# Performance work log

Measured on AMD Instinct MI355X. Metric: run time of the kernel, lower is better.

The kernel has to match this reference:

```python
import jax, jax.numpy as jnp
import numpy as np

C = 64

def conv2d(x, w, b, pad):
    out = jax.lax.conv_general_dilated(x, w, (1, 1), [(pad, pad), (pad, pad)],
                                       dimension_numbers=('NCHW', 'OIHW', 'NCHW'))
    return out + b[None, :, None, None]


def deform_conv(x, w_off, b_off, w, b, pad):
    # Standard pure-pytorch DeformConv2d (offset conv is 3x3/pad1, sampling on
    # zero-padded input, p0 starts at 1, bilinear gather, then kxk weight contraction).
    ks = w.shape[-1]
    N = ks * ks
    B, Cc, H, W = x.shape
    off = conv2d(x, w_off, b_off, 1)                      # (B, 2N, H, W)
    xp = jnp.pad(x, ((0, 0), (0, 0), (pad, pad), (pad, pad))) if pad > 0 else x
    Hp, Wp = xp.shape[2], xp.shape[3]
    off = off.transpose(0, 2, 3, 1)                       # (B, H, W, 2N)
    r = jnp.arange(-(ks - 1) // 2, (ks - 1) // 2 + 1, dtype=x.dtype)
    pn_x = jnp.repeat(r, ks)                              # (N,) kernel row offsets (n = i*ks + j)
    pn_y = jnp.tile(r, ks)                                # (N,) kernel col offsets
    p0_x = jnp.arange(1, H + 1, dtype=x.dtype)[:, None, None]   # (H,1,1)
    p0_y = jnp.arange(1, W + 1, dtype=x.dtype)[:, None]         # (W,1)
    px = off[..., :N] + p0_x + pn_x                       # (B,H,W,N) sample rows
    py = off[..., N:] + p0_y + pn_y                       # (B,H,W,N) sample cols
    fx = jnp.floor(jax.lax.stop_gradient(px))
    fy = jnp.floor(jax.lax.stop_gradient(py))
    lt_x = jnp.clip(fx, 0, Hp - 1)
    lt_y = jnp.clip(fy, 0, Wp - 1)
    rb_x = jnp.clip(fx + 1, 0, Hp - 1)
    rb_y = jnp.clip(fy + 1, 0, Wp - 1)
    pxc = jnp.clip(px, 0, Hp - 1)
    pyc = jnp.clip(py, 0, Wp - 1)
    g_lt = (1 + (lt_x - pxc)) * (1 + (lt_y - pyc))
    g_rb = (1 - (rb_x - pxc)) * (1 - (rb_y - pyc))
    g_lb = (1 + (lt_x - pxc)) * (1 - (rb_y - pyc))
    g_rt = (1 - (rb_x - pxc)) * (1 + (lt_y - pyc))
    xpf = xp.reshape(B, Cc, Hp * Wp)

    def gather(qx, qy):
        idx = (qx * Wp + qy).astype(jnp.int32).reshape(B, 1, -1)
        g = jnp.take_along_axis(xpf, jnp.broadcast_to(idx, (B, Cc, idx.shape[-1])), axis=2)
        return g.reshape(B, Cc, H, W, N)

    x_off = (g_lt[:, None] * gather(lt_x, lt_y) +
             g_rb[:, None] * gather(rb_x, rb_y) +
             g_lb[:, None] * gather(lt_x, rb_y) +
             g_rt[:, None] * gather(rb_x, lt_y))          # (B,C,H,W,N)
    out = jnp.einsum('bchwn,ocn->bohw', x_off, w.reshape(w.shape[0], Cc, N))
    return out + b[None, :, None, None]


def setup_inputs() -> dict:
    key = jax.random.key(0)
    ks_list = [1, 3, 5]
    keys = jax.random.split(key, 32)
    inp = {'x': jax.random.normal(keys[0], (4, C, 96, 96), dtype=jnp.float32)}
    i = 1
    for ks in ks_list:
        N = ks * ks
        inp[f'wo{ks}'] = jax.random.normal(keys[i], (2 * N, C, 3, 3), dtype=jnp.float32) * 0.01; i += 1
        inp[f'bo{ks}'] = jax.random.normal(keys[i], (2 * N,), dtype=jnp.float32) * 0.01; i += 1
        inp[f'w{ks}'] = jax.random.normal(keys[i], (C, C, ks, ks), dtype=jnp.float32) * 0.05; i += 1
        inp[f'b{ks}'] = jax.random.normal(keys[i], (C,), dtype=jnp.float32) * 0.05; i += 1
        inp[f'wa{ks}'] = jax.random.normal(keys[i], (C, C, ks, ks), dtype=jnp.float32) * 0.05; i += 1
        inp[f'ba{ks}'] = jax.random.normal(keys[i], (C,), dtype=jnp.float32) * 0.05; i += 1
    return inp


def reference(x, wo1, bo1, w1, b1, wa1, ba1, wo3, bo3, w3, b3, wa3, ba3, wo5, bo5, w5, b5, wa5, ba5):
    lrelu = lambda t: jnp.where(t >= 0, t, 0.1 * t)
    x1 = lrelu(deform_conv(x, wo1, bo1, w1, b1, 0))
    x2 = lrelu(deform_conv(x, wo3, bo3, w3, b3, 1))
    x3 = lrelu(deform_conv(x, wo5, bo5, w5, b5, 2))
    msf = x1 + x2 + x3
    att = jax.nn.sigmoid(conv2d(msf, wa1, ba1, 0) + conv2d(msf, wa3, ba3, 1) + conv2d(msf, wa5, ba5, 2))
    return msf * att + msf
```

## Files before the change

kernel.cpp:

```cpp
#include <hip/hip_runtime.h>
#include <math.h>

constexpr int B = 4, C = 64, H = 96, W = 96, HW = H * W;

constexpr size_t OFF_OFFALL = 0;
constexpr size_t OFF_MSF    = OFF_OFFALL;
constexpr size_t OFF_X1     = OFF_OFFALL + (size_t)B*72*HW;
constexpr size_t OFF_X2     = OFF_X1  + (size_t)B*64*HW;
constexpr size_t OFF_X3A    = OFF_X2  + (size_t)B*64*HW;
constexpr size_t OFF_X3B    = OFF_X3A + (size_t)B*64*HW;
constexpr size_t OFF_X3C    = OFF_X3B + (size_t)B*64*HW;
constexpr size_t OFF_WOT    = OFF_X3C + (size_t)B*64*HW;
constexpr size_t OFF_BOALL  = OFF_WOT + (size_t)64*9*72;
constexpr size_t OFF_W1T    = OFF_BOALL + 72;
constexpr size_t OFF_W3T    = OFF_W1T + (size_t)64*64;
constexpr size_t OFF_W5T    = OFF_W3T + (size_t)9*64*64;
constexpr size_t OFF_WEFF   = OFF_W5T + (size_t)25*64*64;
constexpr size_t OFF_BEFF   = OFF_WEFF + (size_t)64*25*64;

__global__ void prep_all(const float* __restrict__ wo1, const float* __restrict__ bo1,
                         const float* __restrict__ wo3, const float* __restrict__ bo3,
                         const float* __restrict__ wo5, const float* __restrict__ bo5,
                         const float* __restrict__ w1, const float* __restrict__ w3,
                         const float* __restrict__ w5,
                         const float* __restrict__ wa1, const float* __restrict__ ba1,
                         const float* __restrict__ wa3, const float* __restrict__ ba3,
                         const float* __restrict__ wa5, const float* __restrict__ ba5,
                         float* __restrict__ woT, float* __restrict__ boAll,
                         float* __restrict__ w1T, float* __restrict__ w3T,
                         float* __restrict__ w5T,
                         float* __restrict__ weff, float* __restrict__ beff) {
  int idx = blockIdx.x * 256 + threadIdx.x;
  if (idx < 41472) {
    int ic = idx / (9 * 72), tap = (idx / 72) % 9, oc = idx % 72;
    float v = 0.f;
    if (oc < 2)       v = wo1[(oc * 64 + ic) * 9 + tap];
    else if (oc < 20) v = wo3[((oc - 2) * 64 + ic) * 9 + tap];
    else if (oc < 70) v = wo5[((oc - 20) * 64 + ic) * 9 + tap];
    woT[idx] = v;
  }
  if (idx < 72) boAll[idx] = idx < 2 ? bo1[idx] : idx < 20 ? bo3[idx - 2] : idx < 70 ? bo5[idx - 20] : 0.f;
  if (idx < 64) beff[idx] = ba1[idx] + ba3[idx] + ba5[idx];
  int i2 = idx - 41472;
  if (i2 >= 0 && i2 < 143360) {
    int seg = i2 >> 12, rem = i2 & 4095;
    int c = rem >> 6, o = rem & 63;
    if (seg < 1)       w1T[rem]                     = w1[o * 64 + c];
    else if (seg < 10) w3T[(seg - 1) * 4096 + rem]  = w3[(o * 64 + c) * 9 + (seg - 1)];
    else               w5T[(seg - 10) * 4096 + rem] = w5[(o * 64 + c) * 25 + (seg - 10)];
  }
  int i3 = idx - 41472 - 143360;
  if (i3 >= 0 && i3 < 102400) {
    int ic = i3 / 1600, tap = (i3 / 64) % 25, oc = i3 & 63;
    int kh = tap / 5, kw = tap % 5;
    float v = wa5[(oc * 64 + ic) * 25 + tap];
    if (kh >= 1 && kh <= 3 && kw >= 1 && kw <= 3)
      v += wa3[(oc * 64 + ic) * 9 + (kh - 1) * 3 + (kw - 1)];
    if (tap == 12) v += wa1[oc * 64 + ic];
    weff[i3] = v;
  }
}

__global__ __launch_bounds__(256) void conv_off(const float* __restrict__ x,
                                                const float* __restrict__ woT,
                                                const float* __restrict__ boAll,
                                                float* __restrict__ offAll) {
  __shared__ __align__(16) float xs[8][3][100];
  __shared__ __align__(16) float wsh[8 * 9 * 72];
  const int h = blockIdx.x, b = blockIdx.y;
  const int tid = threadIdx.x;
  const int ocg = tid >> 5, pixg = tid & 31;
  const int oc0 = ocg * 9, w0 = pixg * 3;
  float acc[9][3] = {};

  for (int cc = 0; cc < 8; ++cc) {
    __syncthreads();
    for (int idx = tid; idx < 2400; idx += 256) {
      int ic = idx / 300;
      int r  = (idx / 100) % 3;
      int j  = idx % 100;
      int wc = j - 1, hr = h - 1 + r;
      float v = 0.f;
      if (wc >= 0 && wc < 96 && hr >= 0 && hr < 96)
        v = x[((size_t)(b * 64 + cc * 8 + ic) * 96 + hr) * 96 + wc];
      xs[ic][r][j] = v;
    }
    {
      const float4* src = reinterpret_cast<const float4*>(woT + cc * 5184);
      float4* dst = reinterpret_cast<float4*>(wsh);
      for (int i = tid; i < 1296; i += 256) dst[i] = src[i];
    }
    __syncthreads();
#pragma unroll 2
    for (int ic = 0; ic < 8; ++ic) {
#pragma unroll
      for (int kh = 0; kh < 3; ++kh) {
        float xv[5];
#pragma unroll
        for (int t = 0; t < 5; ++t) xv[t] = xs[ic][kh][w0 + t];
#pragma unroll
        for (int kw = 0; kw < 3; ++kw) {
          const float* wrow = &wsh[(ic * 9 + kh * 3 + kw) * 72 + oc0];
#pragma unroll
          for (int o = 0; o < 9; ++o) {
            float wv = wrow[o];
            acc[o][0] += wv * xv[kw + 0];
            acc[o][1] += wv * xv[kw + 1];
            acc[o][2] += wv * xv[kw + 2];
          }
        }
      }
    }
  }
#pragma unroll
  for (int o = 0; o < 9; ++o) {
    int oc = oc0 + o;
    float bias = boAll[oc];
#pragma unroll
    for (int p = 0; p < 3; ++p)
      offAll[((size_t)(b * 72 + oc) * 96 + h) * 96 + w0 + p] = acc[o][p] + bias;
  }
}

template <int KS>
__device__ __forceinline__ void deform_body(const float* __restrict__ x,
                                            const float* __restrict__ offAll,
                                            const float* __restrict__ wT,
                                            float* __restrict__ dst,
                                            int n0, int n1,
                                            float* __restrict__ xoffn,
                                            float* __restrict__ wn,
                                            int* __restrict__ sp_i,
                                            float* __restrict__ sp_g,
                                            int h, int b, int tid) {
  constexpr int N = KS * KS, P = (KS - 1) / 2, HP = H + 2 * P;
  constexpr int CHB = (KS == 1) ? 0 : (KS == 3) ? 2 : 20;
  const int ocg = tid >> 5, pixg = tid & 31;
  const int oc0 = ocg * 8, w0 = pixg * 3;
  float acc[8][3] = {};
  const float* xb = x + (size_t)b * 64 * HW;

  for (int n = n0; n < n1; ++n) {
    if (tid < 96) {
      int w = tid;
      float ox = offAll[((size_t)(b * 72 + CHB + n) * 96 + h) * 96 + w];
      float oy = offAll[((size_t)(b * 72 + CHB + N + n) * 96 + h) * 96 + w];
      float px = ox + (float)(h + 1 + n / KS - P);
      float py = oy + (float)(w + 1 + n % KS - P);
      float fx = floorf(px), fy = floorf(py);
      float hpm = (float)(HP - 1);
      float ltx = fminf(fmaxf(fx, 0.f), hpm);
      float rbx = fminf(fmaxf(fx + 1.f, 0.f), hpm);
      float lty = fminf(fmaxf(fy, 0.f), hpm);
      float rby = fminf(fmaxf(fy + 1.f, 0.f), hpm);
      float pxc = fminf(fmaxf(px, 0.f), hpm);
      float pyc = fminf(fmaxf(py, 0.f), hpm);
      float gx0 = 1.f + (ltx - pxc);
      float gx1 = 1.f - (rbx - pxc);
      float gy0 = 1.f + (lty - pyc);
      float gy1 = 1.f - (rby - pyc);
      sp_i[0 * 96 + w] = (int)ltx; sp_i[1 * 96 + w] = (int)rbx;
      sp_i[2 * 96 + w] = (int)lty; sp_i[3 * 96 + w] = (int)rby;
      sp_g[0 * 96 + w] = gx0 * gy0;
      sp_g[1 * 96 + w] = gx1 * gy1;
      sp_g[2 * 96 + w] = gx0 * gy1;
      sp_g[3 * 96 + w] = gx1 * gy0;
    }
    __syncthreads();
    for (int cc = 0; cc < 2; ++cc) {
      {
        const float4* src = reinterpret_cast<const float4*>(wT + (size_t)n * 4096 + cc * 2048);
        float4* dw = reinterpret_cast<float4*>(wn);
        dw[tid] = src[tid];
        dw[tid + 256] = src[tid + 256];
      }
#pragma unroll 4
      for (int it = 0; it < 12; ++it) {
        int idx = it * 256 + tid;
        int cl = idx / 96, rp = idx - cl * 96;
        int ix0 = sp_i[0 * 96 + rp], ix1 = sp_i[1 * 96 + rp];
        int iy0 = sp_i[2 * 96 + rp], iy1 = sp_i[3 * 96 + rp];
        const float* xc = xb + (size_t)(cc * 32 + cl) * HW;
        float v00, v11, v01, v10;
        if constexpr (P == 0) {
          v00 = xc[ix0 * 96 + iy0];
          v11 = xc[ix1 * 96 + iy1];
          v01 = xc[ix0 * 96 + iy1];
          v10 = xc[ix1 * 96 + iy0];
        } else {
          int rx0 = ix0 - P, rx1 = ix1 - P, ry0 = iy0 - P, ry1 = iy1 - P;
          bool bx0 = (rx0 >= 0) && (rx0 < 96), bx1 = (rx1 >= 0) && (rx1 < 96);
          bool by0 = (ry0 >= 0) && (ry0 < 96), by1 = (ry1 >= 0) && (ry1 < 96);
          v00 = (bx0 && by0) ? xc[rx0 * 96 + ry0] : 0.f;
          v11 = (bx1 && by1) ? xc[rx1 * 96 + ry1] : 0.f;
          v01 = (bx0 && by1) ? xc[rx0 * 96 + ry1] : 0.f;
          v10 = (bx1 && by0) ? xc[rx1 * 96 + ry0] : 0.f;
        }
        xoffn[idx] = sp_g[0 * 96 + rp] * v00 + sp_g[1 * 96 + rp] * v11 +
                     sp_g[2 * 96 + rp] * v01 + sp_g[3 * 96 + rp] * v10;
      }
      __syncthreads();
#pragma unroll 2
      for (int cl = 0; cl < 32; ++cl) {
        float xv0 = xoffn[cl * 96 + w0];
        float xv1 = xoffn[cl * 96 + w0 + 1];
        float xv2 = xoffn[cl * 96 + w0 + 2];
        const float4* wp = reinterpret_cast<const float4*>(wn + cl * 64 + oc0);
        float4 wa = wp[0], wb = wp[1];
        float wv[8] = {wa.x, wa.y, wa.z, wa.w, wb.x, wb.y, wb.z, wb.w};
#pragma unroll
        for (int o = 0; o < 8; ++o) {
          acc[o][0] += wv[o] * xv0;
          acc[o][1] += wv[o] * xv1;
          acc[o][2] += wv[o] * xv2;
        }
      }
      __syncthreads();
    }
  }
#pragma unroll
  for (int o = 0; o < 8; ++o) {
    int oc = oc0 + o;
    size_t base = ((size_t)(b * 64 + oc) * 96 + h) * 96 + w0;
    dst[base + 0] = acc[o][0];
    dst[base + 1] = acc[o][1];
    dst[base + 2] = acc[o][2];
  }
}

__global__ __launch_bounds__(256, 6) void deform_all(const float* __restrict__ x,
                                                     const float* __restrict__ offAll,
                                                     const float* __restrict__ w1T,
                                                     const float* __restrict__ w3T,
                                                     const float* __restrict__ w5T,
                                                     float* __restrict__ x1,
                                                     float* __restrict__ x2,
                                                     float* __restrict__ x3a,
                                                     float* __restrict__ x3b,
                                                     float* __restrict__ x3c) {
  __shared__ __align__(16) float xoffn[32 * 96];
  __shared__ __align__(16) float wn[32 * 64];
  __shared__ int   sp_i[4 * 96];
  __shared__ float sp_g[4 * 96];
  int bid = blockIdx.x;
  int typ = bid & 3, idx = bid >> 2;
  int h = idx % 96, b = idx / 96;
  int tid = threadIdx.x;
  if (typ == 0)      deform_body<5>(x, offAll, w5T, x3a, 0, 9,  xoffn, wn, sp_i, sp_g, h, b, tid);
  else if (typ == 1) deform_body<5>(x, offAll, w5T, x3b, 9, 17, xoffn, wn, sp_i, sp_g, h, b, tid);
  else if (typ == 2) deform_body<5>(x, offAll, w5T, x3c, 17, 25, xoffn, wn, sp_i, sp_g, h, b, tid);
  else {
    deform_body<3>(x, offAll, w3T, x2, 0, 9, xoffn, wn, sp_i, sp_g, h, b, tid);
    deform_body<1>(x, offAll, w1T, x1, 0, 1, xoffn, wn, sp_i, sp_g, h, b, tid);
  }
}

__global__ __launch_bounds__(256) void msf_build(const float* __restrict__ x1,
                                                 const float* __restrict__ x2,
                                                 const float* __restrict__ x3a,
                                                 const float* __restrict__ x3b,
                                                 const float* __restrict__ x3c,
                                                 const float* __restrict__ b1,
                                                 const float* __restrict__ b3,
                                                 const float* __restrict__ b5,
                                                 float* __restrict__ msf) {
  int i = blockIdx.x * 256 + threadIdx.x;
  int c = (i / 2304) & 63;
  float bb1 = b1[c], bb3 = b3[c], bb5 = b5[c];
  float4 v1 = reinterpret_cast<const float4*>(x1)[i];
  float4 v2 = reinterpret_cast<const float4*>(x2)[i];
  float4 va = reinterpret_cast<const float4*>(x3a)[i];
  float4 vb = reinterpret_cast<const float4*>(x3b)[i];
  float4 vc = reinterpret_cast<const float4*>(x3c)[i];
  float4 m;
  {
    float a1 = v1.x + bb1; a1 = a1 >= 0.f ? a1 : 0.1f * a1;
    float a2 = v2.x + bb3; a2 = a2 >= 0.f ? a2 : 0.1f * a2;
    float a3 = va.x + vb.x + vc.x + bb5; a3 = a3 >= 0.f ? a3 : 0.1f * a3;
    m.x = a1 + a2 + a3;
  }
  {
    float a1 = v1.y + bb1; a1 = a1 >= 0.f ? a1 : 0.1f * a1;
    float a2 = v2.y + bb3; a2 = a2 >= 0.f ? a2 : 0.1f * a2;
    float a3 = va.y + vb.y + vc.y + bb5; a3 = a3 >= 0.f ? a3 : 0.1f * a3;
    m.y = a1 + a2 + a3;
  }
  {
    float a1 = v1.z + bb1; a1 = a1 >= 0.f ? a1 : 0.1f * a1;
    float a2 = v2.z + bb3; a2 = a2 >= 0.f ? a2 : 0.1f * a2;
    float a3 = va.z + vb.z + vc.z + bb5; a3 = a3 >= 0.f ? a3 : 0.1f * a3;
    m.z = a1 + a2 + a3;
  }
  {
    float a1 = v1.w + bb1; a1 = a1 >= 0.f ? a1 : 0.1f * a1;
    float a2 = v2.w + bb3; a2 = a2 >= 0.f ? a2 : 0.1f * a2;
    float a3 = va.w + vb.w + vc.w + bb5; a3 = a3 >= 0.f ? a3 : 0.1f * a3;
    m.w = a1 + a2 + a3;
  }
  reinterpret_cast<float4*>(msf)[i] = m;
}

__global__ __launch_bounds__(128, 2) void att_final(const float* __restrict__ msf,
                                                    const float* __restrict__ weff,
                                                    const float* __restrict__ beff,
                                                    float* __restrict__ out) {
  __shared__ __align__(16) float xs[4 * 5 * 100];
  __shared__ __align__(16) float wsh[4 * 25 * 32];
  const int h = blockIdx.x, b = blockIdx.y, zoc = blockIdx.z * 32;
  const int tid = threadIdx.x;
  const int ocg = tid >> 5, colg = tid & 31;
  const int oc0 = ocg * 8, w0 = colg * 3;
  float acc[8][3] = {};

  for (int cc = 0; cc < 16; ++cc) {
    __syncthreads();
    for (int idx = tid; idx < 2000; idx += 128) {
      int ic = idx / 500, r = (idx / 100) % 5, j = idx % 100;
      int hr = h - 2 + r, wc = j - 2;
      float v = 0.f;
      if (hr >= 0 && hr < 96 && wc >= 0 && wc < 96)
        v = msf[((size_t)(b * 64 + cc * 4 + ic) * 96 + hr) * 96 + wc];
      xs[idx] = v;
    }
    for (int i = tid; i < 800; i += 128) {
      int ict = i >> 3, o4 = i & 7;
      int ic = ict / 25, tap = ict % 25;
      reinterpret_cast<float4*>(wsh)[i] =
          *reinterpret_cast<const float4*>(weff + ((size_t)(cc * 4 + ic) * 25 + tap) * 64 + zoc + o4 * 4);
    }
    __syncthreads();
#pragma unroll
    for (int ic = 0; ic < 4; ++ic) {
#pragma unroll
      for (int kh = 0; kh < 5; ++kh) {
        float xv[7];
#pragma unroll
        for (int t = 0; t < 7; ++t) xv[t] = xs[ic * 500 + kh * 100 + w0 + t];
#pragma unroll
        for (int kw = 0; kw < 5; ++kw) {
          const float4* wp = reinterpret_cast<const float4*>(&wsh[(ic * 25 + kh * 5 + kw) * 32 + oc0]);
          float4 wa = wp[0], wb = wp[1];
          float wv[8] = {wa.x, wa.y, wa.z, wa.w, wb.x, wb.y, wb.z, wb.w};
#pragma unroll
          for (int o = 0; o < 8; ++o) {
            acc[o][0] += wv[o] * xv[kw + 0];
            acc[o][1] += wv[o] * xv[kw + 1];
            acc[o][2] += wv[o] * xv[kw + 2];
          }
        }
      }
    }
  }
#pragma unroll
  for (int o = 0; o < 8; ++o) {
    int oc = zoc + oc0 + o;
    float bz = beff[oc];
#pragma unroll
    for (int p = 0; p < 3; ++p) {
      float z = acc[o][p] + bz;
      float att = 1.f / (1.f + __expf(-z));
      size_t oi = ((size_t)(b * 64 + oc) * 96 + h) * 96 + w0 + p;
      float m = msf[oi];
      out[oi] = m + m * att;
    }
  }
}

extern "C" void kernel_launch(void* const* d_in, const int* in_sizes, int n_in,
                              void* d_out, int out_size, void* d_ws, size_t ws_size,
                              hipStream_t stream) {
  const float* x   = (const float*)d_in[0];
  const float* wo1 = (const float*)d_in[1];
  const float* bo1 = (const float*)d_in[2];
  const float* w1  = (const float*)d_in[3];
  const float* b1  = (const float*)d_in[4];
  const float* wa1 = (const float*)d_in[5];
  const float* ba1 = (const float*)d_in[6];
  const float* wo3 = (const float*)d_in[7];
  const float* bo3 = (const float*)d_in[8];
  const float* w3  = (const float*)d_in[9];
  const float* b3  = (const float*)d_in[10];
  const float* wa3 = (const float*)d_in[11];
  const float* ba3 = (const float*)d_in[12];
  const float* wo5 = (const float*)d_in[13];
  const float* bo5 = (const float*)d_in[14];
  const float* w5  = (const float*)d_in[15];
  const float* b5  = (const float*)d_in[16];
  const float* wa5 = (const float*)d_in[17];
  const float* ba5 = (const float*)d_in[18];

  float* ws     = (float*)d_ws;
  float* offAll = ws + OFF_OFFALL;
  float* msf    = ws + OFF_MSF;
  float* x1     = ws + OFF_X1;
  float* x2     = ws + OFF_X2;
  float* x3a    = ws + OFF_X3A;
  float* x3b    = ws + OFF_X3B;
  float* x3c    = ws + OFF_X3C;
  float* woT    = ws + OFF_WOT;
  float* boAll  = ws + OFF_BOALL;
  float* w1T    = ws + OFF_W1T;
  float* w3T    = ws + OFF_W3T;
  float* w5T    = ws + OFF_W5T;
  float* weff   = ws + OFF_WEFF;
  float* beff   = ws + OFF_BEFF;

  float* out = (float*)d_out;

  hipLaunchKernelGGL(prep_all, dim3(1122), dim3(256), 0, stream,
                     wo1, bo1, wo3, bo3, wo5, bo5, w1, w3, w5,
                     wa1, ba1, wa3, ba3, wa5, ba5,
                     woT, boAll, w1T, w3T, w5T, weff, beff);
  hipLaunchKernelGGL(conv_off, dim3(96, 4), dim3(256), 0, stream, x, woT, boAll, offAll);
  hipLaunchKernelGGL(deform_all, dim3(1536), dim3(256), 0, stream,
                     x, offAll, w1T, w3T, w5T, x1, x2, x3a, x3b, x3c);
  hipLaunchKernelGGL(msf_build, dim3(2304), dim3(256), 0, stream,
                     x1, x2, x3a, x3b, x3c, b1, b3, b5, msf);
  hipLaunchKernelGGL(att_final, dim3(96, 4, 2), dim3(128), 0, stream,
                     msf, weff, beff, out);
}
```

Measured before the change: 750.2 us.

## Move deformable conv contraction to split-bf16 MFMA with padded input and atomics

Replaces the scalar FMA weight contraction in the deformable conv kernels with bf16 MFMA 16x16x32 instructions. Both activations and weights are split into high and low bf16 parts and combined with three MFMAs to keep close to fp32 accuracy. The input is pre-padded into a 100x100 buffer so the bilinear gathers need no bounds checks. The 5x5 branch accumulates its three tap slices atomically into one zeroed buffer instead of three separate buffers. Offset-conv and attention kernels are also split across more blocks along output channels, and the work adds extra pad and zero kernels plus atomic traffic.

```diff
diff --git a/kernel.cpp b/kernel.cpp
--- a/kernel.cpp
+++ b/kernel.cpp
@@ -2,20 +2,23 @@
 #include <math.h>
 
 constexpr int B = 4, C = 64, H = 96, W = 96, HW = H * W;
+constexpr int HWP = 100 * 100;
+
+typedef __attribute__((ext_vector_type(8))) short bf16x8;
+typedef __attribute__((ext_vector_type(4))) float f32x4;
+typedef __attribute__((ext_vector_type(4))) unsigned int uint4v;
 
 constexpr size_t OFF_OFFALL = 0;
-constexpr size_t OFF_MSF    = OFF_OFFALL;
 constexpr size_t OFF_X1     = OFF_OFFALL + (size_t)B*72*HW;
 constexpr size_t OFF_X2     = OFF_X1  + (size_t)B*64*HW;
-constexpr size_t OFF_X3A    = OFF_X2  + (size_t)B*64*HW;
-constexpr size_t OFF_X3B    = OFF_X3A + (size_t)B*64*HW;
-constexpr size_t OFF_X3C    = OFF_X3B + (size_t)B*64*HW;
-constexpr size_t OFF_WOT    = OFF_X3C + (size_t)B*64*HW;
+constexpr size_t OFF_X3     = OFF_X2  + (size_t)B*64*HW;
+constexpr size_t OFF_XPAD   = OFF_X3  + (size_t)B*64*HW;
+constexpr size_t OFF_MSF    = OFF_XPAD;
+constexpr size_t OFF_WOT    = OFF_XPAD + (size_t)B*64*HWP;
 constexpr size_t OFF_BOALL  = OFF_WOT + (size_t)64*9*72;
-constexpr size_t OFF_W1T    = OFF_BOALL + 72;
-constexpr size_t OFF_W3T    = OFF_W1T + (size_t)64*64;
-constexpr size_t OFF_W5T    = OFF_W3T + (size_t)9*64*64;
-constexpr size_t OFF_WEFF   = OFF_W5T + (size_t)25*64*64;
+constexpr size_t OFF_WPKH   = OFF_BOALL + 128;
+constexpr size_t OFF_WPKL   = OFF_WPKH + 71680;
+constexpr size_t OFF_WEFF   = OFF_WPKL + 71680;
 constexpr size_t OFF_BEFF   = OFF_WEFF + (size_t)64*25*64;
 
 __global__ void prep_all(const float* __restrict__ wo1, const float* __restrict__ bo1,
@@ -27,8 +30,7 @@
                          const float* __restrict__ wa3, const float* __restrict__ ba3,
                          const float* __restrict__ wa5, const float* __restrict__ ba5,
                          float* __restrict__ woT, float* __restrict__ boAll,
-                         float* __restrict__ w1T, float* __restrict__ w3T,
-                         float* __restrict__ w5T,
+                         unsigned short* __restrict__ wPkH, unsigned short* __restrict__ wPkL,
                          float* __restrict__ weff, float* __restrict__ beff) {
   int idx = blockIdx.x * 256 + threadIdx.x;
   if (idx < 41472) {
@@ -41,15 +43,7 @@
   }
   if (idx < 72) boAll[idx] = idx < 2 ? bo1[idx] : idx < 20 ? bo3[idx - 2] : idx < 70 ? bo5[idx - 20] : 0.f;
   if (idx < 64) beff[idx] = ba1[idx] + ba3[idx] + ba5[idx];
-  int i2 = idx - 41472;
-  if (i2 >= 0 && i2 < 143360) {
-    int seg = i2 >> 12, rem = i2 & 4095;
-    int c = rem >> 6, o = rem & 63;
-    if (seg < 1)       w1T[rem]                     = w1[o * 64 + c];
-    else if (seg < 10) w3T[(seg - 1) * 4096 + rem]  = w3[(o * 64 + c) * 9 + (seg - 1)];
-    else               w5T[(seg - 10) * 4096 + rem] = w5[(o * 64 + c) * 25 + (seg - 10)];
-  }
-  int i3 = idx - 41472 - 143360;
+  int i3 = idx - 41472;
   if (i3 >= 0 && i3 < 102400) {
     int ic = i3 / 1600, tap = (i3 / 64) % 25, oc = i3 & 63;
     int kh = tap / 5, kw = tap % 5;
@@ -59,36 +53,69 @@
     if (tap == 12) v += wa1[oc * 64 + ic];
     weff[i3] = v;
   }
-}
-
-__global__ __launch_bounds__(256) void conv_off(const float* __restrict__ x,
-                                                const float* __restrict__ woT,
-                                                const float* __restrict__ boAll,
-                                                float* __restrict__ offAll) {
-  __shared__ __align__(16) float xs[8][3][100];
-  __shared__ __align__(16) float wsh[8 * 9 * 72];
-  const int h = blockIdx.x, b = blockIdx.y;
-  const int tid = threadIdx.x;
+  int e = idx - 143872;
+  if (e >= 0 && e < 143360) {
+    int i  = e & 7;
+    int l  = (e >> 3) & 63;
+    int nt = (e >> 9) & 3;
+    int kt = (e >> 11) & 1;
+    int tap = e >> 12;
+    int c  = kt * 32 + 8 * (l >> 4) + i;
+    int oc = nt * 16 + (l & 15);
+    float w;
+    if (tap == 0)      w = w1[oc * 64 + c];
+    else if (tap < 10) w = w3[(oc * 64 + c) * 9 + (tap - 1)];
+    else               w = w5[(oc * 64 + c) * 25 + (tap - 10)];
+    unsigned bits = __float_as_uint(w);
+    unsigned hib  = bits & 0xffff0000u;
+    float lo = w - __uint_as_float(hib);
+    wPkH[e] = (unsigned short)(bits >> 16);
+    wPkL[e] = (unsigned short)(__float_as_uint(lo) >> 16);
+  }
+}
+
+__global__ void pad_x(const float* __restrict__ x, float* __restrict__ xpad) {
+  int i = blockIdx.x * 256 + threadIdx.x;
+  if (i >= B * 64 * HWP) return;
+  int u = i % HWP, bc = i / HWP;
+  int r = u / 100, col = u % 100;
+  float v = 0.f;
+  if (r >= 2 && r < 98 && col >= 2 && col < 98)
+    v = x[(size_t)bc * HW + (r - 2) * 96 + (col - 2)];
+  xpad[i] = v;
+}
+
+__global__ void zero_buf(float* __restrict__ p) {
+  int i = blockIdx.x * 256 + threadIdx.x;
+  reinterpret_cast<float4*>(p)[i] = make_float4(0.f, 0.f, 0.f, 0.f);
+}
+
+template <int NOC, int OCB>
+__device__ __forceinline__ void conv_off_body(const float* __restrict__ x,
+                                              const float* __restrict__ woT,
+                                              const float* __restrict__ boAll,
+                                              float* __restrict__ offAll,
+                                              float* __restrict__ xs,
+                                              float* __restrict__ wsh,
+                                              int h, int b, int tid) {
+  constexpr int OCPG = NOC / 8;
   const int ocg = tid >> 5, pixg = tid & 31;
-  const int oc0 = ocg * 9, w0 = pixg * 3;
-  float acc[9][3] = {};
+  const int oc0 = ocg * OCPG, w0 = pixg * 3;
+  float acc[OCPG][3] = {};
 
   for (int cc = 0; cc < 8; ++cc) {
     __syncthreads();
     for (int idx = tid; idx < 2400; idx += 256) {
-      int ic = idx / 300;
-      int r  = (idx / 100) % 3;
-      int j  = idx % 100;
+      int ic = idx / 300, r = (idx / 100) % 3, j = idx % 100;
       int wc = j - 1, hr = h - 1 + r;
       float v = 0.f;
       if (wc >= 0 && wc < 96 && hr >= 0 && hr < 96)
         v = x[((size_t)(b * 64 + cc * 8 + ic) * 96 + hr) * 96 + wc];
-      xs[ic][r][j] = v;
-    }
-    {
-      const float4* src = reinterpret_cast<const float4*>(woT + cc * 5184);
-      float4* dst = reinterpret_cast<float4*>(wsh);
-      for (int i = tid; i < 1296; i += 256) dst[i] = src[i];
+      xs[(ic * 3 + r) * 100 + j] = v;
+    }
+    for (int i = tid; i < 8 * 9 * NOC; i += 256) {
+      int ic = i / (9 * NOC), rem = i % (9 * NOC), tap = rem / NOC, j = rem % NOC;
+      wsh[i] = woT[((size_t)(cc * 8 + ic) * 9 + tap) * 72 + OCB + j];
     }
     __syncthreads();
 #pragma unroll 2
@@ -97,12 +124,12 @@
       for (int kh = 0; kh < 3; ++kh) {
         float xv[5];
 #pragma unroll
-        for (int t = 0; t < 5; ++t) xv[t] = xs[ic][kh][w0 + t];
+        for (int t = 0; t < 5; ++t) xv[t] = xs[(ic * 3 + kh) * 100 + w0 + t];
 #pragma unroll
         for (int kw = 0; kw < 3; ++kw) {
-          const float* wrow = &wsh[(ic * 9 + kh * 3 + kw) * 72 + oc0];
-#pragma unroll
-          for (int o = 0; o < 9; ++o) {
+          const float* wrow = &wsh[(ic * 9 + kh * 3 + kw) * NOC + oc0];
+#pragma unroll
+          for (int o = 0; o < OCPG; ++o) {
             float wv = wrow[o];
             acc[o][0] += wv * xv[kw + 0];
             acc[o][1] += wv * xv[kw + 1];
@@ -113,8 +140,8 @@
     }
   }
 #pragma unroll
-  for (int o = 0; o < 9; ++o) {
-    int oc = oc0 + o;
+  for (int o = 0; o < OCPG; ++o) {
+    int oc = OCB + oc0 + o;
     float bias = boAll[oc];
 #pragma unroll
     for (int p = 0; p < 3; ++p)
@@ -122,27 +149,40 @@
   }
 }
 
-template <int KS>
-__device__ __forceinline__ void deform_body(const float* __restrict__ x,
-                                            const float* __restrict__ offAll,
-                                            const float* __restrict__ wT,
-                                            float* __restrict__ dst,
-                                            int n0, int n1,
-                                            float* __restrict__ xoffn,
-                                            float* __restrict__ wn,
-                                            int* __restrict__ sp_i,
-                                            float* __restrict__ sp_g,
-                                            int h, int b, int tid) {
-  constexpr int N = KS * KS, P = (KS - 1) / 2, HP = H + 2 * P;
-  constexpr int CHB = (KS == 1) ? 0 : (KS == 3) ? 2 : 20;
-  const int ocg = tid >> 5, pixg = tid & 31;
-  const int oc0 = ocg * 8, w0 = pixg * 3;
-  float acc[8][3] = {};
-  const float* xb = x + (size_t)b * 64 * HW;
+__global__ __launch_bounds__(256) void conv_off(const float* __restrict__ x,
+                                                const float* __restrict__ woT,
+                                                const float* __restrict__ boAll,
+                                                float* __restrict__ offAll) {
+  __shared__ __align__(16) float xs[8 * 3 * 100];
+  __shared__ __align__(16) float wsh[8 * 9 * 40];
+  const int h = blockIdx.x, b = blockIdx.y, tid = threadIdx.x;
+  if (blockIdx.z == 0) conv_off_body<40, 0>(x, woT, boAll, offAll, xs, wsh, h, b, tid);
+  else                 conv_off_body<32, 40>(x, woT, boAll, offAll, xs, wsh, h, b, tid);
+}
+
+template <int KS, bool ATOMIC>
+__device__ __forceinline__ void deform_mfma_body(const float* __restrict__ xpb,
+                                                 const float* __restrict__ offAll,
+                                                 const unsigned short* __restrict__ wPkH,
+                                                 const unsigned short* __restrict__ wPkL,
+                                                 float* __restrict__ dst,
+                                                 int n0, int n1, int b, int h0,
+                                                 int* __restrict__ spb, int* __restrict__ spd,
+                                                 float* __restrict__ spg, int tid) {
+  constexpr int N = KS * KS, P = (KS - 1) / 2, S = 2 - P, HP = H + 2 * P;
+  constexpr int CHB = KS == 1 ? 0 : KS == 3 ? 2 : 20;
+  constexpr int GB  = KS == 1 ? 0 : KS == 3 ? 1 : 10;
+  const int lane = tid & 63, wv = tid >> 6;
+  const int pxw = wv * 48, lg = lane >> 4, lm = lane & 15;
+  f32x4 acc[3][4];
+#pragma unroll
+  for (int a1 = 0; a1 < 3; ++a1)
+#pragma unroll
+    for (int a2 = 0; a2 < 4; ++a2) acc[a1][a2] = (f32x4)0.f;
 
   for (int n = n0; n < n1; ++n) {
-    if (tid < 96) {
-      int w = tid;
+    if (tid < 192) {
+      int w = tid % 96, r = tid / 96, h = h0 + r;
       float ox = offAll[((size_t)(b * 72 + CHB + n) * 96 + h) * 96 + w];
       float oy = offAll[((size_t)(b * 72 + CHB + N + n) * 96 + h) * 96 + w];
       float px = ox + (float)(h + 1 + n / KS - P);
@@ -159,107 +199,112 @@
       float gx1 = 1.f - (rbx - pxc);
       float gy0 = 1.f + (lty - pyc);
       float gy1 = 1.f - (rby - pyc);
-      sp_i[0 * 96 + w] = (int)ltx; sp_i[1 * 96 + w] = (int)rbx;
-      sp_i[2 * 96 + w] = (int)lty; sp_i[3 * 96 + w] = (int)rby;
-      sp_g[0 * 96 + w] = gx0 * gy0;
-      sp_g[1 * 96 + w] = gx1 * gy1;
-      sp_g[2 * 96 + w] = gx0 * gy1;
-      sp_g[3 * 96 + w] = gx1 * gy0;
-    }
-    __syncthreads();
-    for (int cc = 0; cc < 2; ++cc) {
-      {
-        const float4* src = reinterpret_cast<const float4*>(wT + (size_t)n * 4096 + cc * 2048);
-        float4* dw = reinterpret_cast<float4*>(wn);
-        dw[tid] = src[tid];
-        dw[tid + 256] = src[tid + 256];
+      int ix0 = (int)ltx, ix1 = (int)rbx, iy0 = (int)lty, iy1 = (int)rby;
+      spb[tid] = (ix0 + S) * 100 + iy0 + S;
+      spd[tid] = (ix1 - ix0) * 100 + ((iy1 - iy0) << 16);
+      spg[0 * 192 + tid] = gx0 * gy0;
+      spg[1 * 192 + tid] = gx1 * gy1;
+      spg[2 * 192 + tid] = gx0 * gy1;
+      spg[3 * 192 + tid] = gx1 * gy0;
+    }
+    __syncthreads();
+#pragma unroll
+    for (int kt = 0; kt < 2; ++kt) {
+      const int bb = (((GB + n) * 2 + kt)) * 256 + lane;
+      uint4v bh[4], bl[4];
+#pragma unroll
+      for (int nt = 0; nt < 4; ++nt) {
+        bh[nt] = reinterpret_cast<const uint4v*>(wPkH)[bb + nt * 64];
+        bl[nt] = reinterpret_cast<const uint4v*>(wPkL)[bb + nt * 64];
       }
-#pragma unroll 4
-      for (int it = 0; it < 12; ++it) {
-        int idx = it * 256 + tid;
-        int cl = idx / 96, rp = idx - cl * 96;
-        int ix0 = sp_i[0 * 96 + rp], ix1 = sp_i[1 * 96 + rp];
-        int iy0 = sp_i[2 * 96 + rp], iy1 = sp_i[3 * 96 + rp];
-        const float* xc = xb + (size_t)(cc * 32 + cl) * HW;
-        float v00, v11, v01, v10;
-        if constexpr (P == 0) {
-          v00 = xc[ix0 * 96 + iy0];
-          v11 = xc[ix1 * 96 + iy1];
-          v01 = xc[ix0 * 96 + iy1];
-          v10 = xc[ix1 * 96 + iy0];
-        } else {
-          int rx0 = ix0 - P, rx1 = ix1 - P, ry0 = iy0 - P, ry1 = iy1 - P;
-          bool bx0 = (rx0 >= 0) && (rx0 < 96), bx1 = (rx1 >= 0) && (rx1 < 96);
-          bool by0 = (ry0 >= 0) && (ry0 < 96), by1 = (ry1 >= 0) && (ry1 < 96);
-          v00 = (bx0 && by0) ? xc[rx0 * 96 + ry0] : 0.f;
-          v11 = (bx1 && by1) ? xc[rx1 * 96 + ry1] : 0.f;
-          v01 = (bx0 && by1) ? xc[rx0 * 96 + ry1] : 0.f;
-          v10 = (bx1 && by0) ? xc[rx1 * 96 + ry0] : 0.f;
+#pragma unroll
+      for (int mt = 0; mt < 3; ++mt) {
+        int px = pxw + mt * 16 + lm;
+        int base = spb[px];
+        int d = spd[px];
+        int dx = d & 0xffff, dy = d >> 16;
+        float g0 = spg[px], g1 = spg[192 + px], g2 = spg[384 + px], g3 = spg[576 + px];
+        const float* xc = xpb + (kt * 32 + lg * 8) * HWP + base;
+        float vv[8];
+#pragma unroll
+        for (int i = 0; i < 8; ++i) {
+          const float* p = xc + i * HWP;
+          vv[i] = g0 * p[0] + g1 * p[dx + dy] + g2 * p[dy] + g3 * p[dx];
         }
-        xoffn[idx] = sp_g[0 * 96 + rp] * v00 + sp_g[1 * 96 + rp] * v11 +
-                     sp_g[2 * 96 + rp] * v01 + sp_g[3 * 96 + rp] * v10;
-      }
-      __syncthreads();
-#pragma unroll 2
-      for (int cl = 0; cl < 32; ++cl) {
-        float xv0 = xoffn[cl * 96 + w0];
-        float xv1 = xoffn[cl * 96 + w0 + 1];
-        float xv2 = xoffn[cl * 96 + w0 + 2];
-        const float4* wp = reinterpret_cast<const float4*>(wn + cl * 64 + oc0);
-        float4 wa = wp[0], wb = wp[1];
-        float wv[8] = {wa.x, wa.y, wa.z, wa.w, wb.x, wb.y, wb.z, wb.w};
-#pragma unroll
-        for (int o = 0; o < 8; ++o) {
-          acc[o][0] += wv[o] * xv0;
-          acc[o][1] += wv[o] * xv1;
-          acc[o][2] += wv[o] * xv2;
+        unsigned hp[4], lp[4];
+#pragma unroll
+        for (int j = 0; j < 4; ++j) {
+          unsigned b0 = __float_as_uint(vv[2 * j]), b1 = __float_as_uint(vv[2 * j + 1]);
+          unsigned h0b = b0 & 0xffff0000u, h1b = b1 & 0xffff0000u;
+          float l0 = vv[2 * j] - __uint_as_float(h0b);
+          float l1 = vv[2 * j + 1] - __uint_as_float(h1b);
+          hp[j] = (b0 >> 16) | h1b;
+          lp[j] = (__float_as_uint(l0) >> 16) | (__float_as_uint(l1) & 0xffff0000u);
+        }
+        uint4v hv = {hp[0], hp[1], hp[2], hp[3]};
+        uint4v lv = {lp[0], lp[1], lp[2], lp[3]};
+        bf16x8 ah = __builtin_bit_cast(bf16x8, hv);
+        bf16x8 al = __builtin_bit_cast(bf16x8, lv);
+#pragma unroll
+        for (int nt = 0; nt < 4; ++nt) {
+          bf16x8 BH = __builtin_bit_cast(bf16x8, bh[nt]);
+          bf16x8 BL = __builtin_bit_cast(bf16x8, bl[nt]);
+          acc[mt][nt] = __builtin_amdgcn_mfma_f32_16x16x32_bf16(ah, BH, acc[mt][nt], 0, 0, 0);
+          acc[mt][nt] = __builtin_amdgcn_mfma_f32_16x16x32_bf16(al, BH, acc[mt][nt], 0, 0, 0);
+          acc[mt][nt] = __builtin_amdgcn_mfma_f32_16x16x32_bf16(ah, BL, acc[mt][nt], 0, 0, 0);
         }
       }
-      __syncthreads();
-    }
-  }
-#pragma unroll
-  for (int o = 0; o < 8; ++o) {
-    int oc = oc0 + o;
-    size_t base = ((size_t)(b * 64 + oc) * 96 + h) * 96 + w0;
-    dst[base + 0] = acc[o][0];
-    dst[base + 1] = acc[o][1];
-    dst[base + 2] = acc[o][2];
-  }
-}
-
-__global__ __launch_bounds__(256, 6) void deform_all(const float* __restrict__ x,
-                                                     const float* __restrict__ offAll,
-                                                     const float* __restrict__ w1T,
-                                                     const float* __restrict__ w3T,
-                                                     const float* __restrict__ w5T,
-                                                     float* __restrict__ x1,
-                                                     float* __restrict__ x2,
-                                                     float* __restrict__ x3a,
-                                                     float* __restrict__ x3b,
-                                                     float* __restrict__ x3c) {
-  __shared__ __align__(16) float xoffn[32 * 96];
-  __shared__ __align__(16) float wn[32 * 64];
-  __shared__ int   sp_i[4 * 96];
-  __shared__ float sp_g[4 * 96];
+    }
+    __syncthreads();
+  }
+#pragma unroll
+  for (int mt = 0; mt < 3; ++mt) {
+#pragma unroll
+    for (int reg = 0; reg < 4; ++reg) {
+      int px = pxw + mt * 16 + lg * 4 + reg;
+      int rr = px >= 96 ? 1 : 0;
+      int wcol = px - rr * 96;
+#pragma unroll
+      for (int nt = 0; nt < 4; ++nt) {
+        int oc = nt * 16 + lm;
+        size_t ai = ((size_t)(b * 64 + oc) * 96 + h0 + rr) * 96 + wcol;
+        float val = acc[mt][nt][reg];
+        if (ATOMIC) atomicAdd(&dst[ai], val);
+        else        dst[ai] = val;
+      }
+    }
+  }
+}
+
+__global__ __launch_bounds__(256, 3) void deform_mfma(const float* __restrict__ xpad,
+                                                      const float* __restrict__ offAll,
+                                                      const unsigned short* __restrict__ wPkH,
+                                                      const unsigned short* __restrict__ wPkL,
+                                                      float* __restrict__ x1,
+                                                      float* __restrict__ x2,
+                                                      float* __restrict__ x3) {
+  __shared__ int spb[192], spd[192];
+  __shared__ float spg[4 * 192];
   int bid = blockIdx.x;
   int typ = bid & 3, idx = bid >> 2;
-  int h = idx % 96, b = idx / 96;
+  int h0 = (idx % 48) * 2, b = idx / 48;
   int tid = threadIdx.x;
-  if (typ == 0)      deform_body<5>(x, offAll, w5T, x3a, 0, 9,  xoffn, wn, sp_i, sp_g, h, b, tid);
-  else if (typ == 1) deform_body<5>(x, offAll, w5T, x3b, 9, 17, xoffn, wn, sp_i, sp_g, h, b, tid);
-  else if (typ == 2) deform_body<5>(x, offAll, w5T, x3c, 17, 25, xoffn, wn, sp_i, sp_g, h, b, tid);
+  const float* xpb = xpad + (size_t)b * 64 * HWP;
+  if (typ == 0)
+    deform_mfma_body<5, true>(xpb, offAll, wPkH, wPkL, x3, 0, 9, b, h0, spb, spd, spg, tid);
+  else if (typ == 1)
+    deform_mfma_body<5, true>(xpb, offAll, wPkH, wPkL, x3, 9, 17, b, h0, spb, spd, spg, tid);
+  else if (typ == 2)
+    deform_mfma_body<5, true>(xpb, offAll, wPkH, wPkL, x3, 17, 25, b, h0, spb, spd, spg, tid);
   else {
-    deform_body<3>(x, offAll, w3T, x2, 0, 9, xoffn, wn, sp_i, sp_g, h, b, tid);
-    deform_body<1>(x, offAll, w1T, x1, 0, 1, xoffn, wn, sp_i, sp_g, h, b, tid);
+    deform_mfma_body<3, false>(xpb, offAll, wPkH, wPkL, x2, 0, 9, b, h0, spb, spd, spg, tid);
+    deform_mfma_body<1, false>(xpb, offAll, wPkH, wPkL, x1, 0, 1, b, h0, spb, spd, spg, tid);
   }
 }
 
 __global__ __launch_bounds__(256) void msf_build(const float* __restrict__ x1,
                                                  const float* __restrict__ x2,
-                                                 const float* __restrict__ x3a,
-                                                 const float* __restrict__ x3b,
-                                                 const float* __restrict__ x3c,
+                                                 const float* __restrict__ x3,
                                                  const float* __restrict__ b1,
                                                  const float* __restrict__ b3,
                                                  const float* __restrict__ b5,
@@ -269,48 +314,39 @@
   float bb1 = b1[c], bb3 = b3[c], bb5 = b5[c];
   float4 v1 = reinterpret_cast<const float4*>(x1)[i];
   float4 v2 = reinterpret_cast<const float4*>(x2)[i];
-  float4 va = reinterpret_cast<const float4*>(x3a)[i];
-  float4 vb = reinterpret_cast<const float4*>(x3b)[i];
-  float4 vc = reinterpret_cast<const float4*>(x3c)[i];
+  float4 v3 = reinterpret_cast<const float4*>(x3)[i];
   float4 m;
-  {
-    float a1 = v1.x + bb1; a1 = a1 >= 0.f ? a1 : 0.1f * a1;
-    float a2 = v2.x + bb3; a2 = a2 >= 0.f ? a2 : 0.1f * a2;
-    float a3 = va.x + vb.x + vc.x + bb5; a3 = a3 >= 0.f ? a3 : 0.1f * a3;
-    m.x = a1 + a2 + a3;
-  }
-  {
-    float a1 = v1.y + bb1; a1 = a1 >= 0.f ? a1 : 0.1f * a1;
-    float a2 = v2.y + bb3; a2 = a2 >= 0.f ? a2 : 0.1f * a2;
-    float a3 = va.y + vb.y + vc.y + bb5; a3 = a3 >= 0.f ? a3 : 0.1f * a3;
-    m.y = a1 + a2 + a3;
-  }
-  {
-    float a1 = v1.z + bb1; a1 = a1 >= 0.f ? a1 : 0.1f * a1;
-    float a2 = v2.z + bb3; a2 = a2 >= 0.f ? a2 : 0.1f * a2;
-    float a3 = va.z + vb.z + vc.z + bb5; a3 = a3 >= 0.f ? a3 : 0.1f * a3;
-    m.z = a1 + a2 + a3;
-  }
-  {
-    float a1 = v1.w + bb1; a1 = a1 >= 0.f ? a1 : 0.1f * a1;
-    float a2 = v2.w + bb3; a2 = a2 >= 0.f ? a2 : 0.1f * a2;
-    float a3 = va.w + vb.w + vc.w + bb5; a3 = a3 >= 0.f ? a3 : 0.1f * a3;
-    m.w = a1 + a2 + a3;
-  }
+  float a1, a2, a3;
+  a1 = v1.x + bb1; a1 = a1 >= 0.f ? a1 : 0.1f * a1;
+  a2 = v2.x + bb3; a2 = a2 >= 0.f ? a2 : 0.1f * a2;
+  a3 = v3.x + bb5; a3 = a3 >= 0.f ? a3 : 0.1f * a3;
+  m.x = a1 + a2 + a3;
+  a1 = v1.y + bb1; a1 = a1 >= 0.f ? a1 : 0.1f * a1;
+  a2 = v2.y + bb3; a2 = a2 >= 0.f ? a2 : 0.1f * a2;
+  a3 = v3.y + bb5; a3 = a3 >= 0.f ? a3 : 0.1f * a3;
+  m.y = a1 + a2 + a3;
+  a1 = v1.z + bb1; a1 = a1 >= 0.f ? a1 : 0.1f * a1;
+  a2 = v2.z + bb3; a2 = a2 >= 0.f ? a2 : 0.1f * a2;
+  a3 = v3.z + bb5; a3 = a3 >= 0.f ? a3 : 0.1f * a3;
+  m.z = a1 + a2 + a3;
+  a1 = v1.w + bb1; a1 = a1 >= 0.f ? a1 : 0.1f * a1;
+  a2 = v2.w + bb3; a2 = a2 >= 0.f ? a2 : 0.1f * a2;
+  a3 = v3.w + bb5; a3 = a3 >= 0.f ? a3 : 0.1f * a3;
+  m.w = a1 + a2 + a3;
   reinterpret_cast<float4*>(msf)[i] = m;
 }
 
-__global__ __launch_bounds__(128, 2) void att_final(const float* __restrict__ msf,
-                                                    const float* __restrict__ weff,
-                                                    const float* __restrict__ beff,
-                                                    float* __restrict__ out) {
+__global__ __launch_bounds__(128) void att_final(const float* __restrict__ msf,
+                                                 const float* __restrict__ weff,
+                                                 const float* __restrict__ beff,
+                                                 float* __restrict__ out) {
   __shared__ __align__(16) float xs[4 * 5 * 100];
-  __shared__ __align__(16) float wsh[4 * 25 * 32];
-  const int h = blockIdx.x, b = blockIdx.y, zoc = blockIdx.z * 32;
+  __shared__ __align__(16) float wsh[4 * 25 * 16];
+  const int h = blockIdx.x, b = blockIdx.y, zoc = blockIdx.z * 16;
   const int tid = threadIdx.x;
   const int ocg = tid >> 5, colg = tid & 31;
-  const int oc0 = ocg * 8, w0 = colg * 3;
-  float acc[8][3] = {};
+  const int oc0 = ocg * 4, w0 = colg * 3;
+  float acc[4][3] = {};
 
   for (int cc = 0; cc < 16; ++cc) {
     __syncthreads();
@@ -322,11 +358,11 @@
         v = msf[((size_t)(b * 64 + cc * 4 + ic) * 96 + hr) * 96 + wc];
       xs[idx] = v;
     }
-    for (int i = tid; i < 800; i += 128) {
-      int ict = i >> 3, o4 = i & 7;
+    for (int i = tid; i < 400; i += 128) {
+      int ict = i >> 2, q = i & 3;
       int ic = ict / 25, tap = ict % 25;
       reinterpret_cast<float4*>(wsh)[i] =
-          *reinterpret_cast<const float4*>(weff + ((size_t)(cc * 4 + ic) * 25 + tap) * 64 + zoc + o4 * 4);
+          *reinterpret_cast<const float4*>(weff + ((size_t)(cc * 4 + ic) * 25 + tap) * 64 + zoc + q * 4);
     }
     __syncthreads();
 #pragma unroll
@@ -338,21 +374,20 @@
         for (int t = 0; t < 7; ++t) xv[t] = xs[ic * 500 + kh * 100 + w0 + t];
 #pragma unroll
         for (int kw = 0; kw < 5; ++kw) {
-          const float4* wp = reinterpret_cast<const float4*>(&wsh[(ic * 25 + kh * 5 + kw) * 32 + oc0]);
-          float4 wa = wp[0], wb = wp[1];
-          float wv[8] = {wa.x, wa.y, wa.z, wa.w, wb.x, wb.y, wb.z, wb.w};
-#pragma unroll
-          for (int o = 0; o < 8; ++o) {
-            acc[o][0] += wv[o] * xv[kw + 0];
-            acc[o][1] += wv[o] * xv[kw + 1];
-            acc[o][2] += wv[o] * xv[kw + 2];
+          const float4 wv = *reinterpret_cast<const float4*>(&wsh[(ic * 25 + kh * 5 + kw) * 16 + oc0]);
+          float wvv[4] = {wv.x, wv.y, wv.z, wv.w};
+#pragma unroll
+          for (int o = 0; o < 4; ++o) {
+            acc[o][0] += wvv[o] * xv[kw + 0];
+            acc[o][1] += wvv[o] * xv[kw + 1];
+            acc[o][2] += wvv[o] * xv[kw + 2];
           }
         }
       }
     }
   }
 #pragma unroll
-  for (int o = 0; o < 8; ++o) {
+  for (int o = 0; o < 4; ++o) {
     int oc = zoc + oc0 + o;
     float bz = beff[oc];
 #pragma unroll
@@ -391,17 +426,15 @@
 
   float* ws     = (float*)d_ws;
   float* offAll = ws + OFF_OFFALL;
-  float* msf    = ws + OFF_MSF;
   float* x1     = ws + OFF_X1;
   float* x2     = ws + OFF_X2;
-  float* x3a    = ws + OFF_X3A;
-  float* x3b    = ws + OFF_X3B;
-  float* x3c    = ws + OFF_X3C;
+  float* x3     = ws + OFF_X3;
+  float* xpad   = ws + OFF_XPAD;
+  float* msf    = ws + OFF_MSF;
   float* woT    = ws + OFF_WOT;
   float* boAll  = ws + OFF_BOALL;
-  float* w1T    = ws + OFF_W1T;
-  float* w3T    = ws + OFF_W3T;
-  float* w5T    = ws + OFF_W5T;
+  unsigned short* wPkH = (unsigned short*)(ws + OFF_WPKH);
+  unsigned short* wPkL = (unsigned short*)(ws + OFF_WPKL);
   float* weff   = ws + OFF_WEFF;
   float* beff   = ws + OFF_BEFF;
 
@@ -410,12 +443,14 @@
   hipLaunchKernelGGL(prep_all, dim3(1122), dim3(256), 0, stream,
                      wo1, bo1, wo3, bo3, wo5, bo5, w1, w3, w5,
                      wa1, ba1, wa3, ba3, wa5, ba5,
-                     woT, boAll, w1T, w3T, w5T, weff, beff);
-  hipLaunchKernelGGL(conv_off, dim3(96, 4), dim3(256), 0, stream, x, woT, boAll, offAll);
-  hipLaunchKernelGGL(deform_all, dim3(1536), dim3(256), 0, stream,
-                     x, offAll, w1T, w3T, w5T, x1, x2, x3a, x3b, x3c);
+                     woT, boAll, wPkH, wPkL, weff, beff);
+  hipLaunchKernelGGL(pad_x, dim3(10000), dim3(256), 0, stream, x, xpad);
+  hipLaunchKernelGGL(zero_buf, dim3(2304), dim3(256), 0, stream, x3);
+  hipLaunchKernelGGL(conv_off, dim3(96, 4, 2), dim3(256), 0, stream, x, woT, boAll, offAll);
+  hipLaunchKernelGGL(deform_mfma, dim3(768), dim3(256), 0, stream,
+                     xpad, offAll, wPkH, wPkL, x1, x2, x3);
   hipLaunchKernelGGL(msf_build, dim3(2304), dim3(256), 0, stream,
-                     x1, x2, x3a, x3b, x3c, b1, b3, b5, msf);
-  hipLaunchKernelGGL(att_final, dim3(96, 4, 2), dim3(128), 0, stream,
+                     x1, x2, x3, b1, b3, b5, msf);
+  hipLaunchKernelGGL(att_final, dim3(96, 4, 4), dim3(128), 0, stream,
                      msf, weff, beff, out);
 }
```

Result: faster. 705.5 us (-5.9%).
